# Optimization experiments

Hardware: AMD Instinct MI355X
Metric: run time of the kernel (lower is better)

## Reference

```python
import jax, jax.numpy as jnp
import numpy as np

N = 8192
F_IN = 128
N_META = 128
N_EMBED = 128


def setup_inputs() -> dict:
    key = jax.random.key(0)
    k1, k2, k3, k4, k5, k6 = jax.random.split(key, 6)
    X = jax.random.normal(k1, (N, F_IN), dtype=jnp.float32)
    A = jax.random.uniform(k2, (N, N), dtype=jnp.float32)  # dense nonneg adjacency
    s = 1.0 / np.sqrt(F_IN)
    W_embed = jax.random.uniform(k3, (N_EMBED, F_IN), dtype=jnp.float32, minval=-s, maxval=s)
    b_embed = jax.random.uniform(k4, (N_EMBED,), dtype=jnp.float32, minval=-s, maxval=s)
    W_assign = jax.random.uniform(k5, (N_META, F_IN), dtype=jnp.float32, minval=-s, maxval=s)
    b_assign = jax.random.uniform(k6, (N_META,), dtype=jnp.float32, minval=-s, maxval=s)
    return {"X": X, "A": A, "W_embed": W_embed, "b_embed": b_embed,
            "W_assign": W_assign, "b_assign": b_assign}


def reference(X, A, W_embed, b_embed, W_assign, b_assign):
    n = A.shape[0]
    # A_hat = A + I; symmetric normalization D^-1/2 A_hat D^-1/2.
    # (Original builds full diag matrices; result equals row/col scaling.)
    A_hat = A + jnp.eye(n, dtype=A.dtype)
    deg = jnp.sum(A_hat, axis=1)
    d_inv_sqrt = jnp.where(deg > 0, jax.lax.rsqrt(deg), 0.0)
    A_norm = d_inv_sqrt[:, None] * A_hat * d_inv_sqrt[None, :]
    AX = A_norm @ X  # shared by both GCN layers: [N, F]
    z_l = AX @ W_embed.T + b_embed                      # [N, n_embed]
    s_l = jax.nn.softmax(AX @ W_assign.T + b_assign, axis=-1)  # [N, n_meta]
    X_next = s_l.T @ z_l                                 # [n_meta, n_embed]
    A_next = s_l.T @ (A @ s_l)                           # [n_meta, n_meta]
    return (X_next, A_next, s_l)
```

## Files before the change

kernel.cpp:

```cpp
#include <hip/hip_runtime.h>
#include <hip/hip_bf16.h>
#include <cstdint>

typedef short v8s __attribute__((ext_vector_type(8)));
typedef float v4f __attribute__((ext_vector_type(4)));

#define DEV __device__ __forceinline__

DEV unsigned short f2bu(float f) {
  unsigned u = __builtin_bit_cast(unsigned, f);
  u += 0x7fffu + ((u >> 16) & 1u);
  return (unsigned short)(u >> 16);
}

DEV v8s pack8(const float4& a, const float4& b) {
  v8s r;
  r[0] = (short)f2bu(a.x); r[1] = (short)f2bu(a.y);
  r[2] = (short)f2bu(a.z); r[3] = (short)f2bu(a.w);
  r[4] = (short)f2bu(b.x); r[5] = (short)f2bu(b.y);
  r[6] = (short)f2bu(b.z); r[7] = (short)f2bu(b.w);
  return r;
}

DEV void gload16(const unsigned short* g, char* l) {
  __builtin_amdgcn_global_load_lds(
      (const __attribute__((address_space(1))) void*)g,
      (__attribute__((address_space(3))) void*)l, 16, 0, 0);
}

template<bool CVT>
__global__ __launch_bounds__(256)
void k_degcvt(const float* __restrict__ A, float* __restrict__ dinv,
              unsigned short* __restrict__ Abf) {
  const int row = blockIdx.x;
  const float* ar = A + (size_t)row * 8192;
  unsigned short* aw = Abf + (size_t)row * 8192;
  float s = 0.f;
  #pragma unroll
  for (int i = 0; i < 8; ++i) {
    const int c = i * 1024 + threadIdx.x * 4;
    float4 v = *(const float4*)(ar + c);
    s += (v.x + v.y) + (v.z + v.w);
    if constexpr (CVT) {
      uint2 w;
      w.x = (unsigned)f2bu(v.x) | ((unsigned)f2bu(v.y) << 16);
      w.y = (unsigned)f2bu(v.z) | ((unsigned)f2bu(v.w) << 16);
      *(uint2*)(aw + c) = w;
    }
  }
  #pragma unroll
  for (int d = 1; d < 64; d <<= 1) s += __shfl_xor(s, d);
  __shared__ float wsum[4];
  if ((threadIdx.x & 63) == 0) wsum[threadIdx.x >> 6] = s;
  __syncthreads();
  if (threadIdx.x == 0) {
    dinv[row] = rsqrtf(1.0f + ((wsum[0] + wsum[1]) + (wsum[2] + wsum[3])));
  }
}

template<bool SCALE>
__global__ __launch_bounds__(256)
void k_transpose(const float* __restrict__ in, unsigned short* __restrict__ out,
                 const float* __restrict__ dinv) {
  __shared__ float tile[32][129];
  const int j0 = blockIdx.x * 32;
  const int t = threadIdx.x;
  const int r0 = t >> 5, sl = t & 31;
  #pragma unroll
  for (int i = 0; i < 4; ++i) {
    int r = r0 + i * 8;
    float4 v = *(const float4*)(in + (size_t)(j0 + r) * 128 + sl * 4);
    float sc = 1.0f;
    if constexpr (SCALE) sc = dinv[j0 + r];
    tile[r][sl * 4 + 0] = v.x * sc;
    tile[r][sl * 4 + 1] = v.y * sc;
    tile[r][sl * 4 + 2] = v.z * sc;
    tile[r][sl * 4 + 3] = v.w * sc;
  }
  __syncthreads();
  const int c = t >> 1, h = t & 1;
  unsigned short* op = out + (size_t)c * 8192 + j0 + h * 16;
  #pragma unroll
  for (int q = 0; q < 2; ++q) {
    int rb = h * 16 + q * 8;
    uint4 w;
    w.x = (unsigned)f2bu(tile[rb + 0][c]) | ((unsigned)f2bu(tile[rb + 1][c]) << 16);
    w.y = (unsigned)f2bu(tile[rb + 2][c]) | ((unsigned)f2bu(tile[rb + 3][c]) << 16);
    w.z = (unsigned)f2bu(tile[rb + 4][c]) | ((unsigned)f2bu(tile[rb + 5][c]) << 16);
    w.w = (unsigned)f2bu(tile[rb + 6][c]) | ((unsigned)f2bu(tile[rb + 7][c]) << 16);
    *(uint4*)(op + q * 8) = w;
  }
}

__global__ __launch_bounds__(512, 4)
void k_gemm_lds(const unsigned short* __restrict__ Ab16,
                const unsigned short* __restrict__ Bt,
                float* __restrict__ parts) {
  __shared__ alignas(16) char bsm[2][32768];
  const int t = threadIdx.x;
  const int wv = t >> 6, l = t & 63;
  const int rg = wv >> 1, wc = wv & 1;
  const int i0 = blockIdx.x * 128 + rg * 32;
  const int k0 = blockIdx.y * 1024;
  const int lr = l & 15, lq = l >> 4;

  const unsigned short* pA0 = Ab16 + (size_t)(i0 + lr) * 8192 + k0 + lq * 8;
  const unsigned short* pA1 = pA0 + (size_t)16 * 8192;

  const int sc = t >> 4, sk16 = t & 15;
  const int gslot = sk16 ^ (sc & 7);
  const unsigned short* pS = Bt + (size_t)sc * 8192 + k0 + gslot * 8;
  const int wvbase = wv * 1024;

  v4f acc[2][4];
  #pragma unroll
  for (int mt = 0; mt < 2; ++mt)
    #pragma unroll
    for (int nt = 0; nt < 4; ++nt) acc[mt][nt] = (v4f){0.f, 0.f, 0.f, 0.f};

  v8s areg[2][4][2];

  auto stage = [&](int c, int buf) {
    #pragma unroll
    for (int i = 0; i < 4; ++i)
      gload16(pS + (size_t)i * 32 * 8192 + c * 128, bsm[buf] + wvbase + i * 8192);
  };

  stage(0, 0);
  #pragma unroll
  for (int kf = 0; kf < 4; ++kf) {
    areg[0][kf][0] = *(const v8s*)(pA0 + kf * 32);
    areg[0][kf][1] = *(const v8s*)(pA1 + kf * 32);
  }
  __syncthreads();

  #pragma unroll
  for (int c = 0; c < 8; ++c) {
    if (c < 7) {
      stage(c + 1, (c + 1) & 1);
      #pragma unroll
      for (int kf = 0; kf < 4; ++kf) {
        areg[(c + 1) & 1][kf][0] = *(const v8s*)(pA0 + (c + 1) * 128 + kf * 32);
        areg[(c + 1) & 1][kf][1] = *(const v8s*)(pA1 + (c + 1) * 128 + kf * 32);
      }
    }
    #pragma unroll
    for (int ks = 0; ks < 4; ++ks) {
      #pragma unroll
      for (int nt = 0; nt < 4; ++nt) {
        const int col = wc * 64 + nt * 16 + lr;
        const int off = (((col << 8) + ks * 64 + lq * 16) ^ ((col & 7) << 4));
        v8s bf = *(const v8s*)(bsm[c & 1] + off);
        acc[0][nt] = __builtin_amdgcn_mfma_f32_16x16x32_bf16(areg[c & 1][ks][0], bf, acc[0][nt], 0, 0, 0);
        acc[1][nt] = __builtin_amdgcn_mfma_f32_16x16x32_bf16(areg[c & 1][ks][1], bf, acc[1][nt], 0, 0, 0);
      }
    }
    if (c < 7) __syncthreads();
  }

  float* p = parts + (size_t)blockIdx.y * (8192 * 128);
  const int colb = wc * 64;
  #pragma unroll
  for (int mt = 0; mt < 2; ++mt)
    #pragma unroll
    for (int nt = 0; nt < 4; ++nt)
      #pragma unroll
      for (int r = 0; r < 4; ++r)
        p[(size_t)(i0 + mt * 16 + lq * 4 + r) * 128 + colb + nt * 16 + lr] = acc[mt][nt][r];
}

__global__ __launch_bounds__(512)
void k_gemm_f32(const float* __restrict__ Af, const unsigned short* __restrict__ Bt,
                float* __restrict__ parts) {
  constexpr int KSTEPS = 2048 / 32;
  const int t = threadIdx.x;
  const int wv = t >> 6, l = t & 63;
  const int rg = wv >> 1, ch = wv & 1;
  const int i0 = blockIdx.x * 128 + rg * 32;
  const int k0 = blockIdx.y * 2048;
  const int lr = l & 15, lk = (l >> 4) * 8;

  const float* pAf0 = Af + (size_t)(i0 + lr) * 8192 + k0 + lk;
  const float* pAf1 = pAf0 + (size_t)16 * 8192;
  const unsigned short* pB[4];
  #pragma unroll
  for (int nt = 0; nt < 4; ++nt)
    pB[nt] = Bt + (size_t)(ch * 64 + nt * 16 + lr) * 8192 + k0 + lk;

  v4f acc[2][4];
  #pragma unroll
  for (int mt = 0; mt < 2; ++mt)
    #pragma unroll
    for (int nt = 0; nt < 4; ++nt) acc[mt][nt] = (v4f){0.f, 0.f, 0.f, 0.f};

  float4 af_[2][2][2];
  v8s bb[2][4];

  auto loadab = [&](int buf, int k) {
    af_[buf][0][0] = *(const float4*)(pAf0 + k);
    af_[buf][0][1] = *(const float4*)(pAf0 + k + 4);
    af_[buf][1][0] = *(const float4*)(pAf1 + k);
    af_[buf][1][1] = *(const float4*)(pAf1 + k + 4);
    #pragma unroll
    for (int nt = 0; nt < 4; ++nt) bb[buf][nt] = *(const v8s*)(pB[nt] + k);
  };
  auto mfmas = [&](int buf) {
    #pragma unroll
    for (int mt = 0; mt < 2; ++mt) {
      v8s a_ = pack8(af_[buf][mt][0], af_[buf][mt][1]);
      #pragma unroll
      for (int nt = 0; nt < 4; ++nt)
        acc[mt][nt] = __builtin_amdgcn_mfma_f32_16x16x32_bf16(a_, bb[buf][nt], acc[mt][nt], 0, 0, 0);
    }
  };

  loadab(0, 0);
  for (int kt = 0; kt < KSTEPS; kt += 2) {
    loadab(1, (kt + 1) * 32);
    mfmas(0);
    if (kt + 2 < KSTEPS) loadab(0, (kt + 2) * 32);
    mfmas(1);
  }

  float* p = parts + (size_t)blockIdx.y * (8192 * 128);
  const int colb = ch * 64;
  #pragma unroll
  for (int mt = 0; mt < 2; ++mt)
    #pragma unroll
    for (int nt = 0; nt < 4; ++nt)
      #pragma unroll
      for (int r = 0; r < 4; ++r)
        p[(size_t)(i0 + mt * 16 + (l >> 4) * 4 + r) * 128 + colb + nt * 16 + lr] = acc[mt][nt][r];
}

__global__ __launch_bounds__(256)
void k_post1(const float* __restrict__ parts, int nsplit,
             const float* __restrict__ dinv, const float* __restrict__ Xg,
             const float* __restrict__ We, const float* __restrict__ be,
             const float* __restrict__ Wa, const float* __restrict__ ba,
             float* __restrict__ sl_out, unsigned short* __restrict__ slt,
             unsigned short* __restrict__ zlt) {
  __shared__ alignas(16) unsigned short axs[32 * 128];
  __shared__ float lg[32 * 128];
  __shared__ unsigned short sbf[32 * 130];
  __shared__ unsigned short zbf[32 * 130];
  const int t = threadIdx.x;
  const int i0 = blockIdx.x * 32;

  {
    const int r = t >> 3, cg = t & 7;
    const size_t base = (size_t)(i0 + r) * 128 + cg * 16;
    float acc[16];
    #pragma unroll
    for (int q = 0; q < 4; ++q) {
      float4 v = *(const float4*)(parts + base + q * 4);
      acc[q * 4 + 0] = v.x; acc[q * 4 + 1] = v.y;
      acc[q * 4 + 2] = v.z; acc[q * 4 + 3] = v.w;
    }
    for (int s = 1; s < nsplit; ++s) {
      #pragma unroll
      for (int q = 0; q < 4; ++q) {
        float4 v = *(const float4*)(parts + (size_t)s * 1048576 + base + q * 4);
        acc[q * 4 + 0] += v.x; acc[q * 4 + 1] += v.y;
        acc[q * 4 + 2] += v.z; acc[q * 4 + 3] += v.w;
      }
    }
    const float di = dinv[i0 + r];
    unsigned short bx[16];
    #pragma unroll
    for (int q = 0; q < 4; ++q) {
      float4 xv = *(const float4*)(Xg + base + q * 4);
      bx[q * 4 + 0] = f2bu(di * (acc[q * 4 + 0] + di * xv.x));
      bx[q * 4 + 1] = f2bu(di * (acc[q * 4 + 1] + di * xv.y));
      bx[q * 4 + 2] = f2bu(di * (acc[q * 4 + 2] + di * xv.z));
      bx[q * 4 + 3] = f2bu(di * (acc[q * 4 + 3] + di * xv.w));
    }
    char* Ab = (char*)axs;
    const int b0 = (r << 8) + cg * 32, sw = (r & 7) << 4;
    uint4 w0, w1;
    w0.x = (unsigned)bx[0] | ((unsigned)bx[1] << 16);
    w0.y = (unsigned)bx[2] | ((unsigned)bx[3] << 16);
    w0.z = (unsigned)bx[4] | ((unsigned)bx[5] << 16);
    w0.w = (unsigned)bx[6] | ((unsigned)bx[7] << 16);
    w1.x = (unsigned)bx[8] | ((unsigned)bx[9] << 16);
    w1.y = (unsigned)bx[10] | ((unsigned)bx[11] << 16);
    w1.z = (unsigned)bx[12] | ((unsigned)bx[13] << 16);
    w1.w = (unsigned)bx[14] | ((unsigned)bx[15] << 16);
    *(uint4*)(Ab + (b0 ^ sw)) = w0;
    *(uint4*)(Ab + ((b0 + 16) ^ sw)) = w1;
  }
  __syncthreads();

  const int wv = t >> 6, l = t & 63, fr = l & 15;
  {
    v4f zac[2][2], lac[2][2];
    #pragma unroll
    for (int a = 0; a < 2; ++a)
      #pragma unroll
      for (int b = 0; b < 2; ++b) {
        zac[a][b] = (v4f){0.f, 0.f, 0.f, 0.f};
        lac[a][b] = (v4f){0.f, 0.f, 0.f, 0.f};
      }
    const int kk = (l >> 4) * 8;
    #pragma unroll
    for (int ks = 0; ks < 4; ++ks) {
      const int k = ks * 32 + kk;
      #pragma unroll
      for (int nj = 0; nj < 2; ++nj) {
        const int col = nj * 64 + wv * 16 + fr;
        v8s bfe = pack8(*(const float4*)(We + col * 128 + k),
                        *(const float4*)(We + col * 128 + k + 4));
        v8s bfa = pack8(*(const float4*)(Wa + col * 128 + k),
                        *(const float4*)(Wa + col * 128 + k + 4));
        #pragma unroll
        for (int mt = 0; mt < 2; ++mt) {
          const int arow = mt * 16 + fr;
          v8s af = *(const v8s*)((char*)axs + (((arow << 8) + k * 2) ^ ((fr & 7) << 4)));
          zac[mt][nj] = __builtin_amdgcn_mfma_f32_16x16x32_bf16(af, bfe, zac[mt][nj], 0, 0, 0);
          lac[mt][nj] = __builtin_amdgcn_mfma_f32_16x16x32_bf16(af, bfa, lac[mt][nj], 0, 0, 0);
        }
      }
    }
    #pragma unroll
    for (int mt = 0; mt < 2; ++mt)
      #pragma unroll
      for (int nj = 0; nj < 2; ++nj)
        #pragma unroll
        for (int r4 = 0; r4 < 4; ++r4) {
          const int row = mt * 16 + (l >> 4) * 4 + r4;
          const int col = nj * 64 + wv * 16 + fr;
          lg[row * 128 + col] = lac[mt][nj][r4] + ba[col];
          zbf[row * 130 + col] = f2bu(zac[mt][nj][r4] + be[col]);
        }
  }
  __syncthreads();

  {
    const int r = t >> 3, g = t & 7;
    const float* lp = lg + r * 128 + g * 16;
    float x[16];
    #pragma unroll
    for (int q = 0; q < 4; ++q) {
      float4 v = *(const float4*)(lp + q * 4);
      x[q * 4 + 0] = v.x; x[q * 4 + 1] = v.y; x[q * 4 + 2] = v.z; x[q * 4 + 3] = v.w;
    }
    float mx = x[0];
    #pragma unroll
    for (int j = 1; j < 16; ++j) mx = fmaxf(mx, x[j]);
    #pragma unroll
    for (int d = 1; d < 8; d <<= 1) mx = fmaxf(mx, __shfl_xor(mx, d));
    float sum = 0.f;
    #pragma unroll
    for (int j = 0; j < 16; ++j) { x[j] = __expf(x[j] - mx); sum += x[j]; }
    #pragma unroll
    for (int d = 1; d < 8; d <<= 1) sum += __shfl_xor(sum, d);
    const float inv = 1.0f / sum;
    float* op = sl_out + (size_t)(i0 + r) * 128 + g * 16;
    #pragma unroll
    for (int q = 0; q < 4; ++q) {
      float4 o;
      o.x = x[q * 4 + 0] * inv; o.y = x[q * 4 + 1] * inv;
      o.z = x[q * 4 + 2] * inv; o.w = x[q * 4 + 3] * inv;
      *(float4*)(op + q * 4) = o;
    }
    #pragma unroll
    for (int j = 0; j < 16; ++j) sbf[r * 130 + g * 16 + j] = f2bu(x[j] * inv);
  }
  __syncthreads();

  {
    const int c = t & 127;
    const unsigned short* src = (t < 128) ? sbf : zbf;
    unsigned short* dst = (t < 128) ? slt : zlt;
    unsigned short* o = dst + (size_t)c * 8192 + i0;
    #pragma unroll
    for (int q = 0; q < 4; ++q) {
      uint4 w;
      w.x = (unsigned)src[(q * 8 + 0) * 130 + c] | ((unsigned)src[(q * 8 + 1) * 130 + c] << 16);
      w.y = (unsigned)src[(q * 8 + 2) * 130 + c] | ((unsigned)src[(q * 8 + 3) * 130 + c] << 16);
      w.z = (unsigned)src[(q * 8 + 4) * 130 + c] | ((unsigned)src[(q * 8 + 5) * 130 + c] << 16);
      w.w = (unsigned)src[(q * 8 + 6) * 130 + c] | ((unsigned)src[(q * 8 + 7) * 130 + c] << 16);
      *(uint4*)(o + q * 8) = w;
    }
  }
}

__global__ __launch_bounds__(256)
void k_post2(const float* __restrict__ parts, int nsplit, unsigned short* __restrict__ ast) {
  __shared__ unsigned short sb[32 * 130];
  const int t = threadIdx.x;
  const int i0 = blockIdx.x * 32;
  {
    const int r = t >> 3, cg = t & 7;
    const size_t base = (size_t)(i0 + r) * 128 + cg * 16;
    float acc[16];
    #pragma unroll
    for (int q = 0; q < 4; ++q) {
      float4 v = *(const float4*)(parts + base + q * 4);
      acc[q * 4 + 0] = v.x; acc[q * 4 + 1] = v.y;
      acc[q * 4 + 2] = v.z; acc[q * 4 + 3] = v.w;
    }
    for (int s = 1; s < nsplit; ++s) {
      #pragma unroll
      for (int q = 0; q < 4; ++q) {
        float4 v = *(const float4*)(parts + (size_t)s * 1048576 + base + q * 4);
        acc[q * 4 + 0] += v.x; acc[q * 4 + 1] += v.y;
        acc[q * 4 + 2] += v.z; acc[q * 4 + 3] += v.w;
      }
    }
    #pragma unroll
    for (int j = 0; j < 16; ++j) sb[r * 130 + cg * 16 + j] = f2bu(acc[j]);
  }
  __syncthreads();
  if (t < 128) {
    unsigned short* o = ast + (size_t)t * 8192 + i0;
    #pragma unroll
    for (int q = 0; q < 4; ++q) {
      uint4 w;
      w.x = (unsigned)sb[(q * 8 + 0) * 130 + t] | ((unsigned)sb[(q * 8 + 1) * 130 + t] << 16);
      w.y = (unsigned)sb[(q * 8 + 2) * 130 + t] | ((unsigned)sb[(q * 8 + 3) * 130 + t] << 16);
      w.z = (unsigned)sb[(q * 8 + 4) * 130 + t] | ((unsigned)sb[(q * 8 + 5) * 130 + t] << 16);
      w.w = (unsigned)sb[(q * 8 + 6) * 130 + t] | ((unsigned)sb[(q * 8 + 7) * 130 + t] << 16);
      *(uint4*)(o + q * 8) = w;
    }
  }
}

__global__ __launch_bounds__(256)
void k_outer(const unsigned short* __restrict__ slt, const unsigned short* __restrict__ zlt,
             const unsigned short* __restrict__ ast, float* __restrict__ parts) {
  const int t = threadIdx.x, wv = t >> 6, ln = t & 63;
  const int k0 = blockIdx.x * 128;
  const int lm = ln & 15, lk = (ln >> 4) << 3;
  v4f c1[2][8];
  v4f c2[2][8];
  #pragma unroll
  for (int mt = 0; mt < 2; ++mt)
    #pragma unroll
    for (int nt = 0; nt < 8; ++nt) { c1[mt][nt] = (v4f){0.f,0.f,0.f,0.f}; c2[mt][nt] = (v4f){0.f,0.f,0.f,0.f}; }
  #pragma unroll
  for (int ks = 0; ks < 4; ++ks) {
    int k = k0 + ks * 32 + lk;
    v8s a0 = *(const v8s*)(slt + (size_t)(wv * 32 + lm) * 8192 + k);
    v8s a1 = *(const v8s*)(slt + (size_t)(wv * 32 + 16 + lm) * 8192 + k);
    #pragma unroll
    for (int nt = 0; nt < 8; ++nt) {
      v8s bz = *(const v8s*)(zlt + (size_t)(nt * 16 + lm) * 8192 + k);
      v8s bs = *(const v8s*)(ast + (size_t)(nt * 16 + lm) * 8192 + k);
      c1[0][nt] = __builtin_amdgcn_mfma_f32_16x16x32_bf16(a0, bz, c1[0][nt], 0, 0, 0);
      c1[1][nt] = __builtin_amdgcn_mfma_f32_16x16x32_bf16(a1, bz, c1[1][nt], 0, 0, 0);
      c2[0][nt] = __builtin_amdgcn_mfma_f32_16x16x32_bf16(a0, bs, c2[0][nt], 0, 0, 0);
      c2[1][nt] = __builtin_amdgcn_mfma_f32_16x16x32_bf16(a1, bs, c2[1][nt], 0, 0, 0);
    }
  }
  float* p = parts + (size_t)blockIdx.x * 32768;
  #pragma unroll
  for (int mt = 0; mt < 2; ++mt)
    #pragma unroll
    for (int nt = 0; nt < 8; ++nt)
      #pragma unroll
      for (int r = 0; r < 4; ++r) {
        int m = wv * 32 + mt * 16 + ((ln >> 4) << 2) + r;
        int n = nt * 16 + lm;
        p[m * 128 + n] = c1[mt][nt][r];
        p[16384 + m * 128 + n] = c2[mt][nt][r];
      }
}

__global__ __launch_bounds__(256)
void k_reduce(const float* __restrict__ parts, float* __restrict__ out) {
  const int o = blockIdx.x * 256 + threadIdx.x;
  float s = 0.f;
  for (int b = 0; b < 64; ++b) s += parts[(size_t)b * 32768 + o];
  out[o] = s;
}

extern "C" void kernel_launch(void* const* d_in, const int* in_sizes, int n_in,
                              void* d_out, int out_size, void* d_ws, size_t ws_size,
                              hipStream_t stream) {
  (void)in_sizes; (void)n_in; (void)out_size;
  const float* X  = (const float*)d_in[0];
  const float* A  = (const float*)d_in[1];
  const float* We = (const float*)d_in[2];
  const float* be = (const float*)d_in[3];
  const float* Wa = (const float*)d_in[4];
  const float* ba = (const float*)d_in[5];
  float* out = (float*)d_out;
  float* sl = out + 32768;

  char* ws = (char*)d_ws;
  constexpr size_t OFF_XPT  = 32768;
  constexpr size_t OFF_SLT  = OFF_XPT + 2097152;
  constexpr size_t OFF_ZLT  = OFF_SLT + 2097152;
  constexpr size_t OFF_AST  = OFF_ZLT + 2097152;
  constexpr size_t OFF_PART = OFF_AST + 2097152;
  constexpr size_t OFF_ABF  = OFF_PART + 67108864;
  constexpr size_t NEED_ABF = OFF_ABF + 134217728ull;

  float*          dinv = (float*)(ws + 0);
  unsigned short* xpt  = (unsigned short*)(ws + OFF_XPT);
  unsigned short* slt  = (unsigned short*)(ws + OFF_SLT);
  unsigned short* zlt  = (unsigned short*)(ws + OFF_ZLT);
  unsigned short* ast  = (unsigned short*)(ws + OFF_AST);
  float*          part = (float*)(ws + OFF_PART);
  unsigned short* abfp = (unsigned short*)(ws + OFF_ABF);

  const bool abf = ws_size >= NEED_ABF;
  const int  sk  = abf ? 8 : 4;

  if (abf) k_degcvt<true><<<8192, 256, 0, stream>>>(A, dinv, abfp);
  else     k_degcvt<false><<<8192, 256, 0, stream>>>(A, dinv, abfp);

  k_transpose<true><<<256, 256, 0, stream>>>(X, xpt, dinv);

  if (abf) k_gemm_lds<<<dim3(64, 8), 512, 0, stream>>>(abfp, xpt, part);
  else     k_gemm_f32<<<dim3(64, 4), 512, 0, stream>>>(A, xpt, part);

  k_post1<<<256, 256, 0, stream>>>(part, sk, dinv, X, We, be, Wa, ba, sl, slt, zlt);

  if (abf) k_gemm_lds<<<dim3(64, 8), 512, 0, stream>>>(abfp, slt, part);
  else     k_gemm_f32<<<dim3(64, 4), 512, 0, stream>>>(A, slt, part);

  k_post2<<<256, 256, 0, stream>>>(part, sk, ast);
  k_outer<<<64, 256, 0, stream>>>(slt, zlt, ast, part);
  k_reduce<<<128, 256, 0, stream>>>(part, out);
}
```

Measured before the change: 207.1 us.

## Shrink GEMM block tile to 64 rows with smaller K chunks and LDS

Replaces the 512-thread, 128-row GEMM block with a 256-thread, 64-row block that stages 64-wide K chunks (16 iterations instead of 8), halving LDS per block and the A register buffers. The grid doubles to 128x8 blocks, so more blocks fit per CU and more waves are available to hide latency. In exchange, each B tile staged in LDS is reused across half as many rows, which increases B traffic and the number of barriers per block.

```diff
diff --git a/kernel.cpp b/kernel.cpp
--- a/kernel.cpp
+++ b/kernel.cpp
@@ -92,25 +92,28 @@
   }
 }
 
-__global__ __launch_bounds__(512, 4)
-void k_gemm_lds(const unsigned short* __restrict__ Ab16,
-                const unsigned short* __restrict__ Bt,
-                float* __restrict__ parts) {
-  __shared__ alignas(16) char bsm[2][32768];
+__global__ __launch_bounds__(256, 4)
+void k_gemm_v2(const unsigned short* __restrict__ Ab16,
+               const unsigned short* __restrict__ Bt,
+               float* __restrict__ parts) {
+  __shared__ alignas(16) char bsm[2][16384];
   const int t = threadIdx.x;
   const int wv = t >> 6, l = t & 63;
-  const int rg = wv >> 1, wc = wv & 1;
-  const int i0 = blockIdx.x * 128 + rg * 32;
+  const int wr = wv >> 1, wcol = wv & 1;
+  const int i0 = blockIdx.x * 64 + wr * 32;
   const int k0 = blockIdx.y * 1024;
   const int lr = l & 15, lq = l >> 4;
 
   const unsigned short* pA0 = Ab16 + (size_t)(i0 + lr) * 8192 + k0 + lq * 8;
   const unsigned short* pA1 = pA0 + (size_t)16 * 8192;
 
-  const int sc = t >> 4, sk16 = t & 15;
-  const int gslot = sk16 ^ (sc & 7);
-  const unsigned short* pS = Bt + (size_t)sc * 8192 + k0 + gslot * 8;
-  const int wvbase = wv * 1024;
+  const int swz = (l & 7) ^ ((l >> 3) & 7);
+  const unsigned short* pS[4];
+  #pragma unroll
+  for (int i = 0; i < 4; ++i) {
+    const int col = wv * 32 + i * 8 + (l >> 3);
+    pS[i] = Bt + (size_t)col * 8192 + k0 + swz * 8;
+  }
 
   v4f acc[2][4];
   #pragma unroll
@@ -118,48 +121,47 @@
     #pragma unroll
     for (int nt = 0; nt < 4; ++nt) acc[mt][nt] = (v4f){0.f, 0.f, 0.f, 0.f};
 
-  v8s areg[2][4][2];
+  v8s areg[2][2][2];
 
   auto stage = [&](int c, int buf) {
     #pragma unroll
     for (int i = 0; i < 4; ++i)
-      gload16(pS + (size_t)i * 32 * 8192 + c * 128, bsm[buf] + wvbase + i * 8192);
+      gload16(pS[i] + c * 64, bsm[buf] + wv * 4096 + i * 1024);
   };
+  auto loadA = [&](int c, int buf) {
+    #pragma unroll
+    for (int kf = 0; kf < 2; ++kf) {
+      areg[buf][kf][0] = *(const v8s*)(pA0 + c * 64 + kf * 32);
+      areg[buf][kf][1] = *(const v8s*)(pA1 + c * 64 + kf * 32);
+    }
+  };
 
   stage(0, 0);
-  #pragma unroll
-  for (int kf = 0; kf < 4; ++kf) {
-    areg[0][kf][0] = *(const v8s*)(pA0 + kf * 32);
-    areg[0][kf][1] = *(const v8s*)(pA1 + kf * 32);
-  }
-  __syncthreads();
-
-  #pragma unroll
-  for (int c = 0; c < 8; ++c) {
-    if (c < 7) {
+  loadA(0, 0);
+  __syncthreads();
+
+  #pragma unroll
+  for (int c = 0; c < 16; ++c) {
+    if (c < 15) {
       stage(c + 1, (c + 1) & 1);
-      #pragma unroll
-      for (int kf = 0; kf < 4; ++kf) {
-        areg[(c + 1) & 1][kf][0] = *(const v8s*)(pA0 + (c + 1) * 128 + kf * 32);
-        areg[(c + 1) & 1][kf][1] = *(const v8s*)(pA1 + (c + 1) * 128 + kf * 32);
+      loadA(c + 1, (c + 1) & 1);
+    }
+    #pragma unroll
+    for (int kf = 0; kf < 2; ++kf) {
+      #pragma unroll
+      for (int nt = 0; nt < 4; ++nt) {
+        const int col = wcol * 64 + nt * 16 + lr;
+        const int off = ((col << 7) + kf * 64 + lq * 16) ^ ((col & 7) << 4);
+        v8s bf = *(const v8s*)(bsm[c & 1] + off);
+        acc[0][nt] = __builtin_amdgcn_mfma_f32_16x16x32_bf16(areg[c & 1][kf][0], bf, acc[0][nt], 0, 0, 0);
+        acc[1][nt] = __builtin_amdgcn_mfma_f32_16x16x32_bf16(areg[c & 1][kf][1], bf, acc[1][nt], 0, 0, 0);
       }
     }
-    #pragma unroll
-    for (int ks = 0; ks < 4; ++ks) {
-      #pragma unroll
-      for (int nt = 0; nt < 4; ++nt) {
-        const int col = wc * 64 + nt * 16 + lr;
-        const int off = (((col << 8) + ks * 64 + lq * 16) ^ ((col & 7) << 4));
-        v8s bf = *(const v8s*)(bsm[c & 1] + off);
-        acc[0][nt] = __builtin_amdgcn_mfma_f32_16x16x32_bf16(areg[c & 1][ks][0], bf, acc[0][nt], 0, 0, 0);
-        acc[1][nt] = __builtin_amdgcn_mfma_f32_16x16x32_bf16(areg[c & 1][ks][1], bf, acc[1][nt], 0, 0, 0);
-      }
-    }
-    if (c < 7) __syncthreads();
+    if (c < 15) __syncthreads();
   }
 
   float* p = parts + (size_t)blockIdx.y * (8192 * 128);
-  const int colb = wc * 64;
+  const int colb = wcol * 64;
   #pragma unroll
   for (int mt = 0; mt < 2; ++mt)
     #pragma unroll
@@ -513,12 +515,12 @@
 
   k_transpose<true><<<256, 256, 0, stream>>>(X, xpt, dinv);
 
-  if (abf) k_gemm_lds<<<dim3(64, 8), 512, 0, stream>>>(abfp, xpt, part);
+  if (abf) k_gemm_v2<<<dim3(128, 8), 256, 0, stream>>>(abfp, xpt, part);
   else     k_gemm_f32<<<dim3(64, 4), 512, 0, stream>>>(A, xpt, part);
 
   k_post1<<<256, 256, 0, stream>>>(part, sk, dinv, X, We, be, Wa, ba, sl, slt, zlt);
 
-  if (abf) k_gemm_lds<<<dim3(64, 8), 512, 0, stream>>>(abfp, slt, part);
+  if (abf) k_gemm_v2<<<dim3(128, 8), 256, 0, stream>>>(abfp, slt, part);
   else     k_gemm_f32<<<dim3(64, 4), 512, 0, stream>>>(A, slt, part);
 
   k_post2<<<256, 256, 0, stream>>>(part, sk, ast);
```

New measurement: 219.4 us. +5.9%, slower.
